# Optimization experiments

Measured on AMD Instinct MI355X. Metric: run time of the kernel, lower is better.

Reference implementation:

```python
import jax, jax.numpy as jnp
import numpy as np

N_NODES = 50000
N_EDGES = 800000
N_GRAPHS = 256
NEG_SLOPE = 0.2
EPS = 1e-16


def gat_layer(x, W, a_src, a_dst, b, src, dst, num_nodes):
    # x: [N, Cin]; W: [H, Cin, Cout]; a_src/a_dst: [H, Cout]; b: [Cout]
    h = jnp.einsum('nc,hco->nho', x, W)                    # [N, H, Cout]
    e_src = jnp.einsum('nho,ho->nh', h, a_src)             # [N, H]
    e_dst = jnp.einsum('nho,ho->nh', h, a_dst)
    e = jax.nn.leaky_relu(e_src[src] + e_dst[dst], NEG_SLOPE)  # [E, H]
    # softmax over incoming edges of each destination node
    e_max = jax.ops.segment_max(e, dst, num_segments=num_nodes)
    e_max = jnp.where(jnp.isfinite(e_max), e_max, 0.0)
    w = jnp.exp(e - e_max[dst])                            # [E, H]
    denom = jax.ops.segment_sum(w, dst, num_segments=num_nodes)
    alpha = w / (denom[dst] + EPS)                         # [E, H]
    msg = h[src] * alpha[:, :, None]                       # [E, H, Cout]
    out = jax.ops.segment_sum(msg, dst, num_segments=num_nodes)  # [N, H, Cout]
    return out.mean(axis=1) + b                            # head-average (concat=False)


def setup_inputs() -> dict:
    key = jax.random.key(0)
    ks = jax.random.split(key, 16)
    H = 2
    inp = {
        'x': jax.random.normal(ks[0], (N_NODES, 16), dtype=jnp.float32),
        'edge_index': jax.random.randint(ks[1], (2, N_EDGES), 0, N_NODES, dtype=jnp.int64),
        'batch': jnp.sort(jax.random.randint(ks[2], (N_NODES,), 0, N_GRAPHS, dtype=jnp.int64)),
        'fc0_w': jax.random.normal(ks[3], (16, 32), dtype=jnp.float32) * 0.1,
        'fc0_b': jnp.zeros((32,), dtype=jnp.float32),
        'W1': jax.random.normal(ks[4], (H, 32, 64), dtype=jnp.float32) * 0.1,
        'a_src1': jax.random.normal(ks[5], (H, 64), dtype=jnp.float32) * 0.1,
        'a_dst1': jax.random.normal(ks[6], (H, 64), dtype=jnp.float32) * 0.1,
        'b1': jnp.zeros((64,), dtype=jnp.float32),
        'W2': jax.random.normal(ks[7], (H, 64, 128), dtype=jnp.float32) * 0.1,
        'a_src2': jax.random.normal(ks[8], (H, 128), dtype=jnp.float32) * 0.1,
        'a_dst2': jax.random.normal(ks[9], (H, 128), dtype=jnp.float32) * 0.1,
        'b2': jnp.zeros((128,), dtype=jnp.float32),
        'lo_w': jax.random.normal(ks[10], (128, 24), dtype=jnp.float32) * 0.1,
        'lo_b': jnp.zeros((24,), dtype=jnp.float32),
    }
    return inp


def reference(x, edge_index, batch, fc0_w, fc0_b, W1, a_src1, a_dst1, b1,
              W2, a_src2, a_dst2, b2, lo_w, lo_b):
    src, dst = edge_index[0], edge_index[1]
    h = jax.nn.elu(x @ fc0_w + fc0_b)                       # [N, 32]
    h = jax.nn.elu(gat_layer(h, W1, a_src1, a_dst1, b1, src, dst, N_NODES))  # [N, 64]
    h = jax.nn.elu(gat_layer(h, W2, a_src2, a_dst2, b2, src, dst, N_NODES))  # [N, 128]
    # global mean pool over graphs
    sums = jax.ops.segment_sum(h, batch, num_segments=N_GRAPHS)             # [G, 128]
    cnts = jax.ops.segment_sum(jnp.ones((h.shape[0], 1), h.dtype), batch, num_segments=N_GRAPHS)
    pooled = sums / jnp.maximum(cnts, 1.0)
    return pooled @ lo_w + lo_b                              # [G, 24]
```

## Files before the change

### kernel.cpp

```cpp
#include <hip/hip_runtime.h>
#include <hip/hip_fp16.h>
#include <math.h>

#define NEG_SLOPE 0.2f
#define GAT_EPS 1e-16f
#define EPB 4096

__device__ __forceinline__ float elu_f(float x) { return x > 0.f ? x : expm1f(x); }
__device__ __forceinline__ float lrelu_f(float x) { return x > 0.f ? x : NEG_SLOPE * x; }

typedef _Float16 half2v __attribute__((ext_vector_type(2)));
typedef _Float16 half8 __attribute__((ext_vector_type(8)));
typedef float f32x4 __attribute__((ext_vector_type(4)));
typedef float f32x2 __attribute__((ext_vector_type(2)));

__device__ __forceinline__ float fdot2f(unsigned int v, unsigned int a, float acc) {
#if __has_builtin(__builtin_amdgcn_fdot2)
    return __builtin_amdgcn_fdot2(__builtin_bit_cast(half2v, v),
                                  __builtin_bit_cast(half2v, a), acc, false);
#else
    __half2 hv = __builtin_bit_cast(__half2, v);
    __half2 ha = __builtin_bit_cast(__half2, a);
    float2 fv = __half22float2(hv), fa = __half22float2(ha);
    return fmaf(fv.x, fa.x, fmaf(fv.y, fa.y, acc));
#endif
}

__device__ __forceinline__ unsigned int pack_half2(float a, float b) {
    __half2 h = __floats2half2_rn(a, b);
    return __builtin_bit_cast(unsigned int, h);
}

#if __has_builtin(__builtin_amdgcn_cvt_pk_fp8_f32) && __has_builtin(__builtin_amdgcn_cvt_pk_f32_fp8)
#define HW_FP8 1
#endif

__device__ __forceinline__ unsigned int pack_fp8x4(float a, float b, float c, float d) {
#ifdef HW_FP8
    int r = 0;
    r = __builtin_amdgcn_cvt_pk_fp8_f32(a, b, r, false);
    r = __builtin_amdgcn_cvt_pk_fp8_f32(c, d, r, true);
    return (unsigned int)r;
#else
    auto enc = [](float x) -> unsigned int {
        if (x != x) return 0x7f;
        float ax = fabsf(x);
        unsigned int s = x < 0.f ? 0x80u : 0u;
        if (ax < 0.001953125f) {
            int m = (int)(ax * 512.f + 0.5f);
            if (m > 7) m = 7;
            return s | (unsigned int)m;
        }
        if (ax >= 448.f) return s | 0x7e;
        int e; float fr = frexpf(ax, &e);
        int m = (int)(fr * 16.f + 0.5f);
        if (m == 16) { m = 8; e += 1; }
        return s | ((unsigned int)(e + 6) << 3) | (unsigned int)(m - 8);
    };
    return enc(a) | (enc(b) << 8) | (enc(c) << 16) | (enc(d) << 24);
#endif
}

template <bool HI>
__device__ __forceinline__ f32x2 fp8x2_to_f32(unsigned int v) {
#ifdef HW_FP8
    return __builtin_amdgcn_cvt_pk_f32_fp8((int)v, HI);
#else
    auto dec = [](unsigned int b) -> float {
        float s = (b & 0x80) ? -1.f : 1.f;
        int e = (b >> 3) & 0xF, m = b & 7;
        if (e == 0) return s * (float)m * 0.001953125f;
        return s * (8.f + (float)m) * exp2f((float)(e - 10));
    };
    unsigned int sh = HI ? 16 : 0;
    f32x2 r;
    r[0] = dec((v >> sh) & 0xFF);
    r[1] = dec((v >> (sh + 8)) & 0xFF);
    return r;
#endif
}

__device__ __forceinline__ float halfReduceSum(float v) {
    #pragma unroll
    for (int off = 16; off > 0; off >>= 1) v += __shfl_xor(v, off, 64);
    return v;
}
__device__ __forceinline__ float quarterReduceSum(float v) {
    #pragma unroll
    for (int off = 8; off > 0; off >>= 1) v += __shfl_xor(v, off, 64);
    return v;
}

__global__ void init_kernel(float* sums, float* cnts, int N, int G,
        const float* __restrict__ W1, const float* __restrict__ as1, const float* __restrict__ ad1,
        const float* __restrict__ W2, const float* __restrict__ as2, const float* __restrict__ ad2,
        float* __restrict__ wa1, float* __restrict__ wd1,
        float* __restrict__ wa2, float* __restrict__ wd2,
        __half* __restrict__ w2t) {
    int i = blockIdx.x * 256 + threadIdx.x;
    if (i < G * 128) sums[i] = 0.f;
    if (i < G) cnts[i] = 0.f;
    if (blockIdx.x == 1) {
        for (int idx = threadIdx.x; idx < 16384; idx += 256) {
            int c2 = idx >> 6, k = idx & 63;
            w2t[idx] = __float2half(W2[(c2 & 1) * 8192 + k * 128 + (c2 >> 1)]);
        }
    }
    if (blockIdx.x == gridDim.x - 1) {
        int t = threadIdx.x;
        if (t < 64) {
            int h = t >> 5, c = t & 31;
            const float* w = W1 + (h * 32 + c) * 64;
            float sa = 0.f, sd = 0.f;
            for (int o = 0; o < 64; ++o) {
                sa = fmaf(w[o], as1[h * 64 + o], sa);
                sd = fmaf(w[o], ad1[h * 64 + o], sd);
            }
            wa1[t] = sa; wd1[t] = sd;
        } else if (t < 192) {
            int u = t - 64, h = u >> 6, c = u & 63;
            const float* w = W2 + (h * 64 + c) * 128;
            float sa = 0.f, sd = 0.f;
            for (int o = 0; o < 128; ++o) {
                sa = fmaf(w[o], as2[h * 128 + o], sa);
                sd = fmaf(w[o], ad2[h * 128 + o], sd);
            }
            wa2[u] = sa; wd2[u] = sd;
        }
    }
}


__global__ __launch_bounds__(256) void bucket_hist(
        const int* __restrict__ dst, int* __restrict__ bhist,
        int NB, int nbl, int E) {
    __shared__ int lh[256];
    int tid = threadIdx.x;
    lh[tid] = 0;
    __syncthreads();
    int base = blockIdx.x * EPB;
    int lim = E - base; if (lim > EPB) lim = EPB;
    for (int k = tid; k < lim; k += 256)
        atomicAdd(&lh[(unsigned)dst[base + k] >> 8], 1);
    __syncthreads();
    if (tid < NB) bhist[(size_t)tid * nbl + blockIdx.x] = lh[tid];
}

__global__ __launch_bounds__(1024) void bucket_scan(
        int* __restrict__ bhist, int* __restrict__ bstart,
        int* __restrict__ ofsN, int NB, int nbl, int E) {
    __shared__ int stot[256];
    __shared__ int sbs[256];
    int tid = threadIdx.x, lane = tid & 63, wid = tid >> 6;
    if (tid < 256) {
        int t = 0;
        if (tid < NB) {
            const int* p = bhist + (size_t)tid * nbl;
            for (int b = 0; b < nbl; ++b) t += p[b];
        }
        stot[tid] = t;
    }
    __syncthreads();
    if (tid < 64) {
        int carry = 0;
        for (int c = 0; c < 256; c += 64) {
            int v = stot[c + lane];
            int incl = v;
            #pragma unroll
            for (int off = 1; off < 64; off <<= 1) {
                int t = __shfl_up(incl, off, 64);
                if (lane >= off) incl += t;
            }
            sbs[c + lane] = incl - v + carry;
            carry += __shfl(incl, 63, 64);
        }
    }
    __syncthreads();
    if (tid < NB) bstart[tid] = sbs[tid];
    if (tid == 0) { bstart[NB] = E; *ofsN = E; }
    for (int bin = wid; bin < NB; bin += 16) {
        int carry = sbs[bin];
        int* p = bhist + (size_t)bin * nbl;
        for (int c = 0; c < nbl; c += 64) {
            int idx = c + lane;
            int v = (idx < nbl) ? p[idx] : 0;
            int incl = v;
            #pragma unroll
            for (int off = 1; off < 64; off <<= 1) {
                int t = __shfl_up(incl, off, 64);
                if (lane >= off) incl += t;
            }
            if (idx < nbl) p[idx] = incl - v + carry;
            carry += __shfl(incl, 63, 64);
        }
    }
}

__global__ __launch_bounds__(256) void bucket_scatter(
        const int* __restrict__ src, const int* __restrict__ dst,
        const int* __restrict__ bhist, uint2* __restrict__ ebuf,
        int NB, int nbl, int E) {
    __shared__ int lc[256];
    int tid = threadIdx.x;
    if (tid < NB) lc[tid] = bhist[(size_t)tid * nbl + blockIdx.x];
    __syncthreads();
    int base = blockIdx.x * EPB;
    int lim = E - base; if (lim > EPB) lim = EPB;
    for (int k = tid; k < lim; k += 256) {
        int d = dst[base + k];
        int s = src[base + k];
        int pos = atomicAdd(&lc[(unsigned)d >> 8], 1);
        ebuf[pos] = make_uint2((unsigned)s, (unsigned)d);
    }
}

__global__ __launch_bounds__(256) void bucket_csr(
        const uint2* __restrict__ ebuf, const int* __restrict__ bstart,
        const int* __restrict__ batch, float* __restrict__ cnts,
        int* __restrict__ ofs, int* __restrict__ sperm, int N) {
    __shared__ int fh[256];
    __shared__ int wtot[4];
    __shared__ int lc[256];
    int bin = blockIdx.x;
    int tid = threadIdx.x, lane = tid & 63, wid = tid >> 6;
    int ebeg = bstart[bin], eend = bstart[bin + 1];
    fh[tid] = 0;
    __syncthreads();
    for (int i = ebeg + tid; i < eend; i += 256)
        atomicAdd(&fh[ebuf[i].y & 255], 1);
    __syncthreads();
    int v = fh[tid];
    int incl = v;
    #pragma unroll
    for (int off = 1; off < 64; off <<= 1) {
        int t = __shfl_up(incl, off, 64);
        if (lane >= off) incl += t;
    }
    if (lane == 63) wtot[wid] = incl;
    __syncthreads();
    int woff = 0;
    #pragma unroll
    for (int w = 0; w < 4; ++w) if (w < wid) woff += wtot[w];
    int excl = incl - v + woff;
    int d = (bin << 8) + tid;
    if (d < N) ofs[d] = ebeg + excl;
    lc[tid] = excl;
    if (d < N) {
        int b = batch[d];
        int b0 = __shfl(b, 0, 64);
        if (__all(b == b0)) {
            unsigned long long m = __ballot(1);
            if (lane == 0) atomicAdd(&cnts[b], (float)__popcll(m));
        } else {
            atomicAdd(&cnts[b], 1.f);
        }
    }
    __syncthreads();
    for (int i = ebeg + tid; i < eend; i += 256) {
        uint2 e = ebuf[i];
        int pos = atomicAdd(&lc[e.y & 255], 1);
        sperm[ebeg + pos] = (int)e.x;
    }
}

__global__ __launch_bounds__(256) void fused_t1(
        const float* __restrict__ x, const float* __restrict__ w0,
        const float* __restrict__ b0, const float* __restrict__ W1,
        const float* __restrict__ wa1, const float* __restrict__ wd1,
        __half* __restrict__ h1, float* __restrict__ es, float* __restrict__ ed, int N) {
    __shared__ float xs[8 * 16];
    __shared__ float hs[8 * 32];
    __shared__ float ws[4096];
    int n0 = blockIdx.x * 8;
    int tid = threadIdx.x;
    {
        const float4* wv4 = reinterpret_cast<const float4*>(W1);
        float4* ws4 = reinterpret_cast<float4*>(ws);
        #pragma unroll
        for (int i = 0; i < 4; ++i) ws4[tid + i * 256] = wv4[tid + i * 256];
    }
    if (tid < 128) {
        int gi = n0 * 16 + tid;
        xs[tid] = (gi < N * 16) ? x[gi] : 0.f;
    }
    __syncthreads();
    {
        int j = tid >> 5, o = tid & 31;
        float acc = b0[o];
        #pragma unroll
        for (int c = 0; c < 16; ++c) acc = fmaf(xs[j * 16 + c], w0[c * 32 + o], acc);
        hs[j * 32 + o] = elu_f(acc);
    }
    __syncthreads();
    int o = tid & 63, h = (tid >> 6) & 1, nh = tid >> 7;
    float acc[4];
    #pragma unroll
    for (int j = 0; j < 4; ++j) acc[j] = 0.f;
    const float* wp = ws + h * 2048 + o;
    #pragma unroll
    for (int c = 0; c < 32; ++c) {
        float wv = wp[c * 64];
        #pragma unroll
        for (int j = 0; j < 4; ++j) acc[j] = fmaf(hs[(nh * 4 + j) * 32 + c], wv, acc[j]);
    }
    #pragma unroll
    for (int j = 0; j < 4; ++j) {
        int n = n0 + nh * 4 + j;
        if (n < N) h1[(size_t)n * 128 + 2 * o + h] = __float2half(acc[j]);
    }
    if (tid < 32) {
        int n = tid >> 2, r = tid & 3, hh = r >> 1, isd = r & 1;
        const float* wv = (isd ? wd1 : wa1) + hh * 32;
        float s = 0.f;
        #pragma unroll
        for (int c = 0; c < 32; ++c) s = fmaf(hs[n * 32 + c], wv[c], s);
        int nn = n0 + n;
        if (nn < N) { if (isd) ed[nn * 2 + hh] = s; else es[nn * 2 + hh] = s; }
    }
}

__global__ __launch_bounds__(256) void t2_mfma(
        const __half* __restrict__ g1h,
        const __half* __restrict__ w2t,
        unsigned char* __restrict__ h8, int N) {
    __shared__ __half sbuf[16384];
    int tid = threadIdx.x;
    {
        const uint4* srcv = reinterpret_cast<const uint4*>(w2t);
        #pragma unroll
        for (int i = 0; i < 8; ++i) {
            int idx = tid + i * 256;
            int row = idx >> 3;
            int byteoff = (idx * 16) ^ ((row & 7) << 4);
            *reinterpret_cast<uint4*>(reinterpret_cast<char*>(sbuf) + byteoff) = srcv[idx];
        }
    }
    __syncthreads();
    int w = tid >> 6, lane = tid & 63;
    int r = lane & 15, kg = lane >> 4;
    int nodei = blockIdx.x * 64 + w * 16 + r;
    const half8* ap = reinterpret_cast<const half8*>(
        reinterpret_cast<const _Float16*>(g1h) + (size_t)nodei * 64 + kg * 8);

    f32x4 acc[16];
    #pragma unroll
    for (int nf = 0; nf < 16; ++nf) acc[nf] = f32x4{0.f, 0.f, 0.f, 0.f};
    half8 az = {};
    #pragma unroll
    for (int ks = 0; ks < 2; ++ks) {
        half8 a = (nodei < N) ? ap[ks * 4] : az;
        #pragma unroll
        for (int nf = 0; nf < 16; ++nf) {
            int brow = nf * 16 + r;
            int bbyte = (brow * 128 + ks * 64 + kg * 16) ^ ((brow & 7) << 4);
            half8 b = *reinterpret_cast<const half8*>(reinterpret_cast<const char*>(sbuf) + bbyte);
            acc[nf] = __builtin_amdgcn_mfma_f32_16x16x32_f16(a, b, acc[nf], 0, 0, 0);
        }
    }
    #pragma unroll
    for (int q = 0; q < 4; ++q) {
        int n = blockIdx.x * 64 + w * 16 + kg * 4 + q;
        if (n < N) {
            uint4 pk;
            pk.x = pack_fp8x4(acc[0][q],  acc[1][q],  acc[2][q],  acc[3][q]);
            pk.y = pack_fp8x4(acc[4][q],  acc[5][q],  acc[6][q],  acc[7][q]);
            pk.z = pack_fp8x4(acc[8][q],  acc[9][q],  acc[10][q], acc[11][q]);
            pk.w = pack_fp8x4(acc[12][q], acc[13][q], acc[14][q], acc[15][q]);
            *reinterpret_cast<uint4*>(h8 + (size_t)n * 256 + r * 16) = pk;
        }
    }
}

__global__ __launch_bounds__(256) void gat_agg1(
        const int* __restrict__ ofs, const int* __restrict__ sperm,
        const float* __restrict__ es, const float* __restrict__ ed,
        const uint4* __restrict__ h1v, const float* __restrict__ b1,
        const float* __restrict__ wa2, const float* __restrict__ wd2,
        uint2* __restrict__ g1h, float* __restrict__ es2, float* __restrict__ ed2, int N) {
    __shared__ uint2 meta[16][32];
    int q = threadIdx.x >> 4;
    int d = blockIdx.x * 16 + q;
    int lane = threadIdx.x & 15;
    bool active = d < N;
    if (!active) return;
    float2 edv = *reinterpret_cast<const float2*>(ed + (size_t)d * 2);
    int beg = ofs[d], end = ofs[d + 1];
    int deg = end - beg;
    int jmax = deg < 32 ? deg : 32;

    int s0i = 0, s1i = 0;
    float ex00 = 0.f, ex01 = 0.f, ex10 = 0.f, ex11 = 0.f;
    int i0 = beg + lane, i1 = beg + lane + 16;
    if (i0 < end) {
        s0i = sperm[i0];
        float2 e = *reinterpret_cast<const float2*>(es + (size_t)s0i * 2);
        ex00 = __expf(lrelu_f(e.x + edv.x));
        ex01 = __expf(lrelu_f(e.y + edv.y));
    }
    if (i1 < end) {
        s1i = sperm[i1];
        float2 e = *reinterpret_cast<const float2*>(es + (size_t)s1i * 2);
        ex10 = __expf(lrelu_f(e.x + edv.x));
        ex11 = __expf(lrelu_f(e.y + edv.y));
    }
    float s0 = ex00 + ex10, s1 = ex01 + ex11;
    for (int i = i0 + 32; i < end; i += 16) {
        int s = sperm[i];
        float2 e = *reinterpret_cast<const float2*>(es + (size_t)s * 2);
        s0 += __expf(lrelu_f(e.x + edv.x));
        s1 += __expf(lrelu_f(e.y + edv.y));
    }
    s0 = quarterReduceSum(s0);
    s1 = quarterReduceSum(s1);
    float r0 = 0.5f / (s0 + GAT_EPS), r1 = 0.5f / (s1 + GAT_EPS);
    if (lane < jmax)
        meta[q][lane] = make_uint2((unsigned int)s0i, pack_half2(ex00 * r0, ex01 * r1));
    if (lane + 16 < jmax)
        meta[q][lane + 16] = make_uint2((unsigned int)s1i, pack_half2(ex10 * r0, ex11 * r1));

    float a0 = 0.f, a1 = 0.f, a2 = 0.f, a3 = 0.f;
    int j = 0;
    for (; j + 8 <= jmax; j += 8) {
        uint4 vv[8];
        #pragma unroll
        for (int k = 0; k < 8; ++k) vv[k] = h1v[(size_t)meta[q][j + k].x * 16 + lane];
        #pragma unroll
        for (int k = 0; k < 8; ++k) {
            unsigned int my = meta[q][j + k].y;
            a0 = fdot2f(vv[k].x, my, a0);
            a1 = fdot2f(vv[k].y, my, a1);
            a2 = fdot2f(vv[k].z, my, a2);
            a3 = fdot2f(vv[k].w, my, a3);
        }
    }
    for (; j + 4 <= jmax; j += 4) {
        uint4 vv[4];
        #pragma unroll
        for (int k = 0; k < 4; ++k) vv[k] = h1v[(size_t)meta[q][j + k].x * 16 + lane];
        #pragma unroll
        for (int k = 0; k < 4; ++k) {
            unsigned int my = meta[q][j + k].y;
            a0 = fdot2f(vv[k].x, my, a0);
            a1 = fdot2f(vv[k].y, my, a1);
            a2 = fdot2f(vv[k].z, my, a2);
            a3 = fdot2f(vv[k].w, my, a3);
        }
    }
    for (; j < jmax; ++j) {
        uint2 m = meta[q][j];
        uint4 v = h1v[(size_t)m.x * 16 + lane];
        a0 = fdot2f(v.x, m.y, a0);
        a1 = fdot2f(v.y, m.y, a1);
        a2 = fdot2f(v.z, m.y, a2);
        a3 = fdot2f(v.w, m.y, a3);
    }
    for (int i = beg + 32; i < end; ++i) {
        int s = sperm[i];
        float2 e = *reinterpret_cast<const float2*>(es + (size_t)s * 2);
        float w0 = __expf(lrelu_f(e.x + edv.x)) * r0;
        float w1 = __expf(lrelu_f(e.y + edv.y)) * r1;
        unsigned int ap = pack_half2(w0, w1);
        uint4 v = h1v[(size_t)s * 16 + lane];
        a0 = fdot2f(v.x, ap, a0);
        a1 = fdot2f(v.y, ap, a1);
        a2 = fdot2f(v.z, ap, a2);
        a3 = fdot2f(v.w, ap, a3);
    }
    float4 bv = reinterpret_cast<const float4*>(b1)[lane];
    float o0 = elu_f(a0 + bv.x);
    float o1 = elu_f(a1 + bv.y);
    float o2 = elu_f(a2 + bv.z);
    float o3 = elu_f(a3 + bv.w);
    g1h[(size_t)d * 16 + lane] = make_uint2(pack_half2(o0, o1), pack_half2(o2, o3));
    float4 wa0 = reinterpret_cast<const float4*>(wa2)[lane];
    float4 wa1v = reinterpret_cast<const float4*>(wa2)[16 + lane];
    float4 wd0 = reinterpret_cast<const float4*>(wd2)[lane];
    float4 wd1v = reinterpret_cast<const float4*>(wd2)[16 + lane];
    float p0 = o0 * wa0.x + o1 * wa0.y + o2 * wa0.z + o3 * wa0.w;
    float p1 = o0 * wa1v.x + o1 * wa1v.y + o2 * wa1v.z + o3 * wa1v.w;
    float q0 = o0 * wd0.x + o1 * wd0.y + o2 * wd0.z + o3 * wd0.w;
    float q1 = o0 * wd1v.x + o1 * wd1v.y + o2 * wd1v.z + o3 * wd1v.w;
    p0 = quarterReduceSum(p0);
    p1 = quarterReduceSum(p1);
    q0 = quarterReduceSum(q0);
    q1 = quarterReduceSum(q1);
    if (lane == 0) {
        es2[(size_t)d * 2]     = p0;
        es2[(size_t)d * 2 + 1] = p1;
        ed2[(size_t)d * 2]     = q0;
        ed2[(size_t)d * 2 + 1] = q1;
    }
}

__global__ __launch_bounds__(256) void gat_agg2(
        const int* __restrict__ ofs, const int* __restrict__ sperm,
        const float* __restrict__ es, const float* __restrict__ ed,
        const uint2* __restrict__ h8v, const float* __restrict__ b2,
        const int* __restrict__ batch, float* __restrict__ sums, int N) {
    __shared__ uint2 meta[8][32];
    __shared__ float louts[8 * 128];
    __shared__ int lbat[8];
    int half = threadIdx.x >> 5;
    int d = blockIdx.x * 8 + half;
    int lane = threadIdx.x & 31;
    bool active = d < N;
    int beg = 0, end = 0;
    if (active) {
        beg = ofs[d]; end = ofs[d + 1];
        if (lane == 0) lbat[half] = batch[d];
    } else if (lane == 0) {
        lbat[half] = -1;
    }
    float2 edv = active ? *reinterpret_cast<const float2*>(ed + (size_t)d * 2)
                        : make_float2(0.f, 0.f);
    int deg = end - beg;
    int jmax = deg < 32 ? deg : 32;

    int s_f = 0;
    float ex0 = 0.f, ex1 = 0.f;
    int i0 = beg + lane;
    if (i0 < end) {
        s_f = sperm[i0];
        float2 esv = *reinterpret_cast<const float2*>(es + (size_t)s_f * 2);
        ex0 = __expf(lrelu_f(esv.x + edv.x));
        ex1 = __expf(lrelu_f(esv.y + edv.y));
    }
    float s0 = ex0, s1 = ex1;
    for (int i = i0 + 32; i < end; i += 32) {
        int s = sperm[i];
        float2 esv = *reinterpret_cast<const float2*>(es + (size_t)s * 2);
        s0 += __expf(lrelu_f(esv.x + edv.x));
        s1 += __expf(lrelu_f(esv.y + edv.y));
    }
    s0 = halfReduceSum(s0);
    s1 = halfReduceSum(s1);
    float r0 = 0.5f / (s0 + GAT_EPS), r1 = 0.5f / (s1 + GAT_EPS);
    if (lane < jmax)
        meta[half][lane] = make_uint2((unsigned int)s_f, pack_half2(ex0 * r0, ex1 * r1));

    int head = (lane >> 1) & 1;
    float acc[8];
    #pragma unroll
    for (int i = 0; i < 8; ++i) acc[i] = 0.f;

    int j = 0;
    for (; j + 8 <= jmax; j += 8) {
        uint2 vv[8];
        #pragma unroll
        for (int k = 0; k < 8; ++k) vv[k] = h8v[(size_t)meta[half][j + k].x * 32 + lane];
        #pragma unroll
        for (int k = 0; k < 8; ++k) {
            __half2 ah = __builtin_bit_cast(__half2, meta[half][j + k].y);
            float2 af = __half22float2(ah);
            float av = head ? af.y : af.x;
            f32x2 f01 = fp8x2_to_f32<false>(vv[k].x);
            f32x2 f23 = fp8x2_to_f32<true>(vv[k].x);
            f32x2 f45 = fp8x2_to_f32<false>(vv[k].y);
            f32x2 f67 = fp8x2_to_f32<true>(vv[k].y);
            acc[0] = fmaf(av, f01[0], acc[0]);
            acc[1] = fmaf(av, f01[1], acc[1]);
            acc[2] = fmaf(av, f23[0], acc[2]);
            acc[3] = fmaf(av, f23[1], acc[3]);
            acc[4] = fmaf(av, f45[0], acc[4]);
            acc[5] = fmaf(av, f45[1], acc[5]);
            acc[6] = fmaf(av, f67[0], acc[6]);
            acc[7] = fmaf(av, f67[1], acc[7]);
        }
    }
    for (; j < jmax; ++j) {
        uint2 v = h8v[(size_t)meta[half][j].x * 32 + lane];
        __half2 ah = __builtin_bit_cast(__half2, meta[half][j].y);
        float2 af = __half22float2(ah);
        float av = head ? af.y : af.x;
        f32x2 f01 = fp8x2_to_f32<false>(v.x);
        f32x2 f23 = fp8x2_to_f32<true>(v.x);
        f32x2 f45 = fp8x2_to_f32<false>(v.y);
        f32x2 f67 = fp8x2_to_f32<true>(v.y);
        acc[0] = fmaf(av, f01[0], acc[0]);
        acc[1] = fmaf(av, f01[1], acc[1]);
        acc[2] = fmaf(av, f23[0], acc[2]);
        acc[3] = fmaf(av, f23[1], acc[3]);
        acc[4] = fmaf(av, f45[0], acc[4]);
        acc[5] = fmaf(av, f45[1], acc[5]);
        acc[6] = fmaf(av, f67[0], acc[6]);
        acc[7] = fmaf(av, f67[1], acc[7]);
    }
    for (int i = beg + 32; i < end; ++i) {
        int s = sperm[i];
        float2 esv = *reinterpret_cast<const float2*>(es + (size_t)s * 2);
        float a0 = __expf(lrelu_f(esv.x + edv.x)) * r0;
        float a1 = __expf(lrelu_f(esv.y + edv.y)) * r1;
        float av = head ? a1 : a0;
        uint2 v = h8v[(size_t)s * 32 + lane];
        f32x2 f01 = fp8x2_to_f32<false>(v.x);
        f32x2 f23 = fp8x2_to_f32<true>(v.x);
        f32x2 f45 = fp8x2_to_f32<false>(v.y);
        f32x2 f67 = fp8x2_to_f32<true>(v.y);
        acc[0] = fmaf(av, f01[0], acc[0]);
        acc[1] = fmaf(av, f01[1], acc[1]);
        acc[2] = fmaf(av, f23[0], acc[2]);
        acc[3] = fmaf(av, f23[1], acc[3]);
        acc[4] = fmaf(av, f45[0], acc[4]);
        acc[5] = fmaf(av, f45[1], acc[5]);
        acc[6] = fmaf(av, f67[0], acc[6]);
        acc[7] = fmaf(av, f67[1], acc[7]);
    }
    #pragma unroll
    for (int i = 0; i < 8; ++i) acc[i] += __shfl_xor(acc[i], 2, 64);
    if (head == 0) {
        int jch = lane >> 2;
        int nfb = (lane & 1) * 8;
        #pragma unroll
        for (int i = 0; i < 8; ++i) {
            int o = (nfb + i) * 8 + jch;
            louts[half * 128 + o] = active ? elu_f(acc[i] + b2[o]) : 0.f;
        }
    }
    __syncthreads();
    if (threadIdx.x < 128) {
        int c = threadIdx.x;
        int cur = lbat[0];
        float a = 0.f;
        #pragma unroll
        for (int n = 0; n < 8; ++n) {
            int b = lbat[n];
            if (b != cur) {
                if (cur >= 0) atomicAdd(&sums[(size_t)cur * 128 + c], a);
                a = 0.f; cur = b;
            }
            a += louts[n * 128 + c];
        }
        if (cur >= 0) atomicAdd(&sums[(size_t)cur * 128 + c], a);
    }
}

__global__ void final_kernel(
        const float* __restrict__ sums, const float* __restrict__ cnts,
        const float* __restrict__ w, const float* __restrict__ b,
        float* __restrict__ out, int G) {
    int g = blockIdx.x;
    int k = threadIdx.x;
    if (k >= 24) return;
    float inv = 1.f / fmaxf(cnts[g], 1.f);
    float acc = b[k];
    #pragma unroll
    for (int c = 0; c < 128; ++c) acc = fmaf(sums[g * 128 + c] * inv, w[c * 24 + k], acc);
    out[g * 24 + k] = acc;
}

extern "C" void kernel_launch(void* const* d_in, const int* in_sizes, int n_in,
                              void* d_out, int out_size, void* d_ws, size_t ws_size,
                              hipStream_t stream) {
    const float* x      = (const float*)d_in[0];
    const int*   ei     = (const int*)d_in[1];
    const int*   batch  = (const int*)d_in[2];
    const float* fc0_w  = (const float*)d_in[3];
    const float* fc0_b  = (const float*)d_in[4];
    const float* W1     = (const float*)d_in[5];
    const float* a_src1 = (const float*)d_in[6];
    const float* a_dst1 = (const float*)d_in[7];
    const float* b1     = (const float*)d_in[8];
    const float* W2     = (const float*)d_in[9];
    const float* a_src2 = (const float*)d_in[10];
    const float* a_dst2 = (const float*)d_in[11];
    const float* b2     = (const float*)d_in[12];
    const float* lo_w   = (const float*)d_in[13];
    const float* lo_b   = (const float*)d_in[14];
    float* out = (float*)d_out;

    const int N = in_sizes[0] / 16;
    const int E = in_sizes[1] / 2;
    const int G = out_size / 24;
    const int* src = ei;
    const int* dst = ei + E;
    const int NB  = (N + 255) >> 8;
    const int nbl = (E + EPB - 1) / EPB;

    char* wsb = (char*)d_ws;
    size_t off = 0;
    auto allocf = [&](size_t n) { float* p = (float*)(wsb + off); off += ((n * 4 + 255) & ~(size_t)255); return p; };
    auto alloci = [&](size_t n) { int* p = (int*)(wsb + off); off += ((n * 4 + 255) & ~(size_t)255); return p; };
    auto alloch = [&](size_t n) { __half* p = (__half*)(wsb + off); off += ((n * 2 + 255) & ~(size_t)255); return p; };
    __half* hbuf  = alloch((size_t)N * 256);
    __half* g1h   = alloch((size_t)(N + 64) * 64);
    __half* w2t   = alloch(16384);
    float*  es    = allocf((size_t)N * 2);
    float*  ed    = allocf((size_t)N * 2);
    float*  es2   = allocf((size_t)N * 2);
    float*  ed2   = allocf((size_t)N * 2);
    float*  sums  = allocf((size_t)G * 128);
    float*  cnts  = allocf((size_t)G);
    float*  wa1   = allocf(64);
    float*  wd1   = allocf(64);
    float*  wa2   = allocf(128);
    float*  wd2   = allocf(128);
    int* ofs     = alloci((size_t)N + 1);
    int* sperm   = alloci((size_t)E);
    int* bhist   = alloci((size_t)NB * nbl);
    int* bstart  = alloci((size_t)NB + 1);
    uint2* ebuf  = (uint2*)alloci((size_t)E * 2);
    (void)ws_size;

    init_kernel<<<(N + 255) / 256, 256, 0, stream>>>(sums, cnts, N, G,
            W1, a_src1, a_dst1, W2, a_src2, a_dst2, wa1, wd1, wa2, wd2, w2t);
    bucket_hist<<<nbl, 256, 0, stream>>>(dst, bhist, NB, nbl, E);
    bucket_scan<<<1, 1024, 0, stream>>>(bhist, bstart, ofs + N, NB, nbl, E);
    bucket_scatter<<<nbl, 256, 0, stream>>>(src, dst, bhist, ebuf, NB, nbl, E);
    bucket_csr<<<NB, 256, 0, stream>>>(ebuf, bstart, batch, cnts, ofs, sperm, N);

    fused_t1<<<(N + 7) / 8, 256, 0, stream>>>(x, fc0_w, fc0_b, W1, wa1, wd1, hbuf, es, ed, N);
    gat_agg1<<<(N + 15) / 16, 256, 0, stream>>>(ofs, sperm, es, ed, (const uint4*)hbuf, b1,
            wa2, wd2, (uint2*)g1h, es2, ed2, N);

    t2_mfma<<<(N + 63) / 64, 256, 0, stream>>>(g1h, w2t, (unsigned char*)hbuf, N);
    gat_agg2<<<(N + 7) / 8, 256, 0, stream>>>(ofs, sperm, es2, ed2, (const uint2*)hbuf, b2,
            batch, sums, N);

    final_kernel<<<G, 32, 0, stream>>>(sums, cnts, lo_w, lo_b, out, G);
}
```

Before: 300.4 us.

## Store layer-1 features as FP8 and parallelize setup reductions

Layer-1 projected features are now staged in shared memory and written as packed FP8 instead of FP16. The first aggregation kernel gathers half as many bytes per edge and decodes FP8 to float before accumulating. Separately, the weight-vector precompute and the bucket-histogram totals are split across several threads with shuffle reductions, and the edges-per-block constant is doubled. The FP8 storage lowers precision of the gathered features and adds conversion instructions in the gather loop.

```diff
diff --git a/kernel.cpp b/kernel.cpp
--- a/kernel.cpp
+++ b/kernel.cpp
@@ -4,7 +4,7 @@
 
 #define NEG_SLOPE 0.2f
 #define GAT_EPS 1e-16f
-#define EPB 4096
+#define EPB 8192
 
 __device__ __forceinline__ float elu_f(float x) { return x > 0.f ? x : expm1f(x); }
 __device__ __forceinline__ float lrelu_f(float x) { return x > 0.f ? x : NEG_SLOPE * x; }
@@ -80,6 +80,18 @@
 #endif
 }
 
+__device__ __forceinline__ void acc8_fp8(uint2 v, float aw0, float aw1,
+        float& a0, float& a1, float& a2, float& a3) {
+    f32x2 f01 = fp8x2_to_f32<false>(v.x);
+    f32x2 f23 = fp8x2_to_f32<true >(v.x);
+    f32x2 f45 = fp8x2_to_f32<false>(v.y);
+    f32x2 f67 = fp8x2_to_f32<true >(v.y);
+    a0 = fmaf(aw0, f01[0], a0); a0 = fmaf(aw1, f01[1], a0);
+    a1 = fmaf(aw0, f23[0], a1); a1 = fmaf(aw1, f23[1], a1);
+    a2 = fmaf(aw0, f45[0], a2); a2 = fmaf(aw1, f45[1], a2);
+    a3 = fmaf(aw0, f67[0], a3); a3 = fmaf(aw1, f67[1], a3);
+}
+
 __device__ __forceinline__ float halfReduceSum(float v) {
     #pragma unroll
     for (int off = 16; off > 0; off >>= 1) v += __shfl_xor(v, off, 64);
@@ -108,24 +120,32 @@
     }
     if (blockIdx.x == gridDim.x - 1) {
         int t = threadIdx.x;
-        if (t < 64) {
-            int h = t >> 5, c = t & 31;
+        {
+            int idx = t >> 2, part = t & 3;
+            int h = idx >> 5, c = idx & 31;
             const float* w = W1 + (h * 32 + c) * 64;
             float sa = 0.f, sd = 0.f;
-            for (int o = 0; o < 64; ++o) {
+            #pragma unroll
+            for (int o = part * 16; o < part * 16 + 16; ++o) {
                 sa = fmaf(w[o], as1[h * 64 + o], sa);
                 sd = fmaf(w[o], ad1[h * 64 + o], sd);
             }
-            wa1[t] = sa; wd1[t] = sd;
-        } else if (t < 192) {
-            int u = t - 64, h = u >> 6, c = u & 63;
+            sa += __shfl_xor(sa, 1, 64); sa += __shfl_xor(sa, 2, 64);
+            sd += __shfl_xor(sd, 1, 64); sd += __shfl_xor(sd, 2, 64);
+            if (part == 0) { wa1[idx] = sa; wd1[idx] = sd; }
+        }
+        {
+            int idx = t >> 1, part = t & 1;
+            int h = idx >> 6, c = idx & 63;
             const float* w = W2 + (h * 64 + c) * 128;
             float sa = 0.f, sd = 0.f;
-            for (int o = 0; o < 128; ++o) {
+            for (int o = part * 64; o < part * 64 + 64; ++o) {
                 sa = fmaf(w[o], as2[h * 128 + o], sa);
                 sd = fmaf(w[o], ad2[h * 128 + o], sd);
             }
-            wa2[u] = sa; wd2[u] = sd;
+            sa += __shfl_xor(sa, 1, 64);
+            sd += __shfl_xor(sd, 1, 64);
+            if (part == 0) { wa2[idx] = sa; wd2[idx] = sd; }
         }
     }
 }
@@ -152,13 +172,16 @@
     __shared__ int stot[256];
     __shared__ int sbs[256];
     int tid = threadIdx.x, lane = tid & 63, wid = tid >> 6;
-    if (tid < 256) {
+    {
+        int bin = tid >> 2, part = tid & 3;
         int t = 0;
-        if (tid < NB) {
-            const int* p = bhist + (size_t)tid * nbl;
-            for (int b = 0; b < nbl; ++b) t += p[b];
-        }
-        stot[tid] = t;
+        if (bin < NB) {
+            const int* p = bhist + (size_t)bin * nbl;
+            for (int b = part; b < nbl; b += 4) t += p[b];
+        }
+        t += __shfl_xor(t, 1, 64);
+        t += __shfl_xor(t, 2, 64);
+        if (part == 0) stot[bin] = t;
     }
     __syncthreads();
     if (tid < 64) {
@@ -267,10 +290,11 @@
         const float* __restrict__ x, const float* __restrict__ w0,
         const float* __restrict__ b0, const float* __restrict__ W1,
         const float* __restrict__ wa1, const float* __restrict__ wd1,
-        __half* __restrict__ h1, float* __restrict__ es, float* __restrict__ ed, int N) {
+        unsigned char* __restrict__ h1, float* __restrict__ es, float* __restrict__ ed, int N) {
     __shared__ float xs[8 * 16];
     __shared__ float hs[8 * 32];
     __shared__ float ws[4096];
+    __shared__ float hs2[8 * 128];
     int n0 = blockIdx.x * 8;
     int tid = threadIdx.x;
     {
@@ -304,10 +328,8 @@
         for (int j = 0; j < 4; ++j) acc[j] = fmaf(hs[(nh * 4 + j) * 32 + c], wv, acc[j]);
     }
     #pragma unroll
-    for (int j = 0; j < 4; ++j) {
-        int n = n0 + nh * 4 + j;
-        if (n < N) h1[(size_t)n * 128 + 2 * o + h] = __float2half(acc[j]);
-    }
+    for (int j = 0; j < 4; ++j)
+        hs2[(nh * 4 + j) * 128 + 2 * o + h] = acc[j];
     if (tid < 32) {
         int n = tid >> 2, r = tid & 3, hh = r >> 1, isd = r & 1;
         const float* wv = (isd ? wd1 : wa1) + hh * 32;
@@ -316,6 +338,18 @@
         for (int c = 0; c < 32; ++c) s = fmaf(hs[n * 32 + c], wv[c], s);
         int nn = n0 + n;
         if (nn < N) { if (isd) ed[nn * 2 + hh] = s; else es[nn * 2 + hh] = s; }
+    }
+    __syncthreads();
+    if (tid < 128) {
+        int nloc = tid >> 4, cg = tid & 15;
+        int n = n0 + nloc;
+        if (n < N) {
+            const float* p = hs2 + nloc * 128 + cg * 8;
+            uint2 pk;
+            pk.x = pack_fp8x4(p[0], p[1], p[2], p[3]);
+            pk.y = pack_fp8x4(p[4], p[5], p[6], p[7]);
+            *reinterpret_cast<uint2*>(h1 + (size_t)n * 128 + cg * 8) = pk;
+        }
     }
 }
 
@@ -374,7 +408,7 @@
 __global__ __launch_bounds__(256) void gat_agg1(
         const int* __restrict__ ofs, const int* __restrict__ sperm,
         const float* __restrict__ es, const float* __restrict__ ed,
-        const uint4* __restrict__ h1v, const float* __restrict__ b1,
+        const uint2* __restrict__ h1v, const float* __restrict__ b1,
         const float* __restrict__ wa2, const float* __restrict__ wd2,
         uint2* __restrict__ g1h, float* __restrict__ es2, float* __restrict__ ed2, int N) {
     __shared__ uint2 meta[16][32];
@@ -421,50 +455,36 @@
     float a0 = 0.f, a1 = 0.f, a2 = 0.f, a3 = 0.f;
     int j = 0;
     for (; j + 8 <= jmax; j += 8) {
-        uint4 vv[8];
+        uint2 vv[8];
         #pragma unroll
         for (int k = 0; k < 8; ++k) vv[k] = h1v[(size_t)meta[q][j + k].x * 16 + lane];
         #pragma unroll
         for (int k = 0; k < 8; ++k) {
-            unsigned int my = meta[q][j + k].y;
-            a0 = fdot2f(vv[k].x, my, a0);
-            a1 = fdot2f(vv[k].y, my, a1);
-            a2 = fdot2f(vv[k].z, my, a2);
-            a3 = fdot2f(vv[k].w, my, a3);
+            float2 af = __half22float2(__builtin_bit_cast(__half2, meta[q][j + k].y));
+            acc8_fp8(vv[k], af.x, af.y, a0, a1, a2, a3);
         }
     }
     for (; j + 4 <= jmax; j += 4) {
-        uint4 vv[4];
+        uint2 vv[4];
         #pragma unroll
         for (int k = 0; k < 4; ++k) vv[k] = h1v[(size_t)meta[q][j + k].x * 16 + lane];
         #pragma unroll
         for (int k = 0; k < 4; ++k) {
-            unsigned int my = meta[q][j + k].y;
-            a0 = fdot2f(vv[k].x, my, a0);
-            a1 = fdot2f(vv[k].y, my, a1);
-            a2 = fdot2f(vv[k].z, my, a2);
-            a3 = fdot2f(vv[k].w, my, a3);
+            float2 af = __half22float2(__builtin_bit_cast(__half2, meta[q][j + k].y));
+            acc8_fp8(vv[k], af.x, af.y, a0, a1, a2, a3);
         }
     }
     for (; j < jmax; ++j) {
         uint2 m = meta[q][j];
-        uint4 v = h1v[(size_t)m.x * 16 + lane];
-        a0 = fdot2f(v.x, m.y, a0);
-        a1 = fdot2f(v.y, m.y, a1);
-        a2 = fdot2f(v.z, m.y, a2);
-        a3 = fdot2f(v.w, m.y, a3);
+        float2 af = __half22float2(__builtin_bit_cast(__half2, m.y));
+        acc8_fp8(h1v[(size_t)m.x * 16 + lane], af.x, af.y, a0, a1, a2, a3);
     }
     for (int i = beg + 32; i < end; ++i) {
         int s = sperm[i];
         float2 e = *reinterpret_cast<const float2*>(es + (size_t)s * 2);
         float w0 = __expf(lrelu_f(e.x + edv.x)) * r0;
         float w1 = __expf(lrelu_f(e.y + edv.y)) * r1;
-        unsigned int ap = pack_half2(w0, w1);
-        uint4 v = h1v[(size_t)s * 16 + lane];
-        a0 = fdot2f(v.x, ap, a0);
-        a1 = fdot2f(v.y, ap, a1);
-        a2 = fdot2f(v.z, ap, a2);
-        a3 = fdot2f(v.w, ap, a3);
+        acc8_fp8(h1v[(size_t)s * 16 + lane], w0, w1, a0, a1, a2, a3);
     }
     float4 bv = reinterpret_cast<const float4*>(b1)[lane];
     float o0 = elu_f(a0 + bv.x);
@@ -708,8 +728,9 @@
     bucket_scatter<<<nbl, 256, 0, stream>>>(src, dst, bhist, ebuf, NB, nbl, E);
     bucket_csr<<<NB, 256, 0, stream>>>(ebuf, bstart, batch, cnts, ofs, sperm, N);
 
-    fused_t1<<<(N + 7) / 8, 256, 0, stream>>>(x, fc0_w, fc0_b, W1, wa1, wd1, hbuf, es, ed, N);
-    gat_agg1<<<(N + 15) / 16, 256, 0, stream>>>(ofs, sperm, es, ed, (const uint4*)hbuf, b1,
+    fused_t1<<<(N + 7) / 8, 256, 0, stream>>>(x, fc0_w, fc0_b, W1, wa1, wd1,
+            (unsigned char*)hbuf, es, ed, N);
+    gat_agg1<<<(N + 15) / 16, 256, 0, stream>>>(ofs, sperm, es, ed, (const uint2*)hbuf, b1,
             wa2, wd2, (uint2*)g1h, es2, ed2, N);
 
     t2_mfma<<<(N + 63) / 64, 256, 0, stream>>>(g1h, w2t, (unsigned char*)hbuf, N);
```

New measurement: 264.8 us. 11.9% less time.
